# Kernel optimization log

Hardware: AMD Instinct MI355X
Metric: run time of the kernel (lower is better)

The kernel has to match this reference:

```python
import math
import jax, jax.numpy as jnp
import numpy as np

B, H, S, D = 2, 16, 2048, 64

def setup_inputs() -> dict:
    key = jax.random.key(0)
    kq, kk, kv, km = jax.random.split(key, 4)
    q = jax.random.normal(kq, (B, H, S, D), dtype=jnp.float32)
    k = jax.random.normal(kk, (B, H, S, D), dtype=jnp.float32)
    v = jax.random.normal(kv, (B, H, S, D), dtype=jnp.float32)
    mask = jax.random.randint(km, (B, S, S), 0, 2, dtype=jnp.int32)
    return {"q": q, "k": k, "v": v, "mask": mask}

def reference(q, k, v, mask):
    # attn = q @ (k^T / sqrt(d))  -> [B,H,Sq,Sk]
    scale = 1.0 / math.sqrt(q.shape[-1])
    attn = jnp.einsum("bhqd,bhkd->bhqk", q, k * scale)
    # masked_fill where mask.unsqueeze(1) == 1
    attn = jnp.where(mask[:, None, :, :] == 1, jnp.float32(-1e9), attn)
    attn = jax.nn.softmax(attn, axis=-1)
    # dropout is identity in eval / p=0
    res = jnp.einsum("bhqk,bhkd->bhqd", attn, v)
    return (res, attn)
```

## Files before the change

kernel.cpp:

```cpp
#include <hip/hip_runtime.h>

#define B_ 2
#define H_ 16
#define S_ 2048
#define D_ 64
#define QB 32
#define KT 64
#define NT (S_ / KT)
#define NTHREADS 512

typedef _Float16 f16;
typedef _Float16 f16x8 __attribute__((ext_vector_type(8)));
typedef _Float16 f16x4 __attribute__((ext_vector_type(4)));
typedef _Float16 f16x2 __attribute__((ext_vector_type(2)));
typedef float f32x4 __attribute__((ext_vector_type(4)));

#define MFMA16(a, b, c) __builtin_amdgcn_mfma_f32_16x16x32_f16(a, b, c, 0, 0, 0)

__global__ __launch_bounds__(NTHREADS)
void attn_kernel(const float* __restrict__ q, const float* __restrict__ k,
                 const float* __restrict__ v, const int* __restrict__ mask,
                 float* __restrict__ out)
{
    __shared__ f16 Qsh[QB][D_ + 8];
    __shared__ f16 Ksh[2][KT][D_ + 8];
    __shared__ f16 Vt [2][D_][KT + 8];
    __shared__ f16 Psh[2][QB][KT + 8];
    __shared__ float rowred[QB];
    __shared__ float rlsh[QB];

    const int tid  = threadIdx.x;
    const int wave = tid >> 6;
    const int lane = tid & 63;
    const int quad = lane >> 4;
    const int l16  = lane & 15;
    const int qi   = wave & 1;
    const int ni   = wave >> 1;

    const int qb = blockIdx.x;
    const int h  = blockIdx.y;
    const int b  = blockIdx.z;
    const int bh = b * H_ + h;

    const float* Qg = q + ((size_t)bh * S_ + (size_t)qb * QB) * D_;
    const float* Kg = k + (size_t)bh * S_ * D_;
    const float* Vg = v + (size_t)bh * S_ * D_;
    const int*   Mg = mask + ((size_t)b * S_ + (size_t)qb * QB) * S_;
    float* res_out  = out + ((size_t)bh * S_ + (size_t)qb * QB) * D_;
    float* attn_out = out + (size_t)B_ * H_ * S_ * D_
                          + ((size_t)bh * S_ + (size_t)qb * QB) * S_;

    if (tid < QB) rowred[tid] = 0.f;

    {
        const int row = tid >> 4;
        const int c4  = (tid & 15) * 4;
        const float4 qv = *(const float4*)(Qg + row * D_ + c4);
        f16x4 o;
        o[0] = (f16)(qv.x * 0.125f); o[1] = (f16)(qv.y * 0.125f);
        o[2] = (f16)(qv.z * 0.125f); o[3] = (f16)(qv.w * 0.125f);
        *(f16x4*)&Qsh[row][c4] = o;
    }

    const int skk = tid >> 3;
    const int sd0 = (tid & 7) * 8;
    const int vkp = tid & 31;
    const int vd0 = (tid >> 5) * 4;

    const int qrow0   = qi * 16 + quad * 4;
    const int colbase = ni * 16 + l16;
    const int* mp0 = Mg + (size_t)qrow0 * S_ + colbase;

    {
        const float* src = Kg + (size_t)skk * D_ + sd0;
        const float4 x0 = *(const float4*)(src);
        const float4 x1 = *(const float4*)(src + 4);
        f16x8 o;
        o[0] = (f16)x0.x; o[1] = (f16)x0.y; o[2] = (f16)x0.z; o[3] = (f16)x0.w;
        o[4] = (f16)x1.x; o[5] = (f16)x1.y; o[6] = (f16)x1.z; o[7] = (f16)x1.w;
        *(f16x8*)&Ksh[0][skk][sd0] = o;
    }
    int mnext[4];
#pragma unroll
    for (int r = 0; r < 4; ++r) mnext[r] = mp0[(size_t)r * S_];
    __syncthreads();

    const f16x8 a0 = *(const f16x8*)&Qsh[qi * 16 + l16][quad * 8];
    const f16x8 a1 = *(const f16x8*)&Qsh[qi * 16 + l16][32 + quad * 8];

    float psum[4] = {0.f, 0.f, 0.f, 0.f};
    for (int kt = 0; kt < NT; ++kt) {
        const int cur = kt & 1;
        const int ktn = (kt + 1 < NT) ? kt + 1 : kt;
        const float* srck = Kg + ((size_t)(ktn * KT + skk)) * D_ + sd0;
        const float4 x0 = *(const float4*)(srck);
        const float4 x1 = *(const float4*)(srck + 4);
        int mcur[4];
#pragma unroll
        for (int r = 0; r < 4; ++r) mcur[r] = mnext[r];
        const int* mpn = mp0 + ktn * KT;
#pragma unroll
        for (int r = 0; r < 4; ++r) mnext[r] = mpn[(size_t)r * S_];

        const f16x8 b0 = *(const f16x8*)&Ksh[cur][ni * 16 + l16][quad * 8];
        const f16x8 b1 = *(const f16x8*)&Ksh[cur][ni * 16 + l16][32 + quad * 8];
        f32x4 c = {0.f, 0.f, 0.f, 0.f};
        c = MFMA16(a0, b0, c);
        c = MFMA16(a1, b1, c);
#pragma unroll
        for (int r = 0; r < 4; ++r)
            psum[r] += (mcur[r] == 1) ? 0.f : __expf(c[r]);

        {
            f16x8 o;
            o[0] = (f16)x0.x; o[1] = (f16)x0.y; o[2] = (f16)x0.z; o[3] = (f16)x0.w;
            o[4] = (f16)x1.x; o[5] = (f16)x1.y; o[6] = (f16)x1.z; o[7] = (f16)x1.w;
            *(f16x8*)&Ksh[cur ^ 1][skk][sd0] = o;
        }
        __syncthreads();
    }

#pragma unroll
    for (int r = 0; r < 4; ++r) {
        psum[r] += __shfl_xor(psum[r], 1);
        psum[r] += __shfl_xor(psum[r], 2);
        psum[r] += __shfl_xor(psum[r], 4);
        psum[r] += __shfl_xor(psum[r], 8);
    }
    if (l16 == 0) {
#pragma unroll
        for (int r = 0; r < 4; ++r) atomicAdd(&rowred[qrow0 + r], psum[r]);
    }
    __syncthreads();
    if (tid < QB) rlsh[tid] = 1.0f / rowred[tid];
    __syncthreads();
    float rlq[4];
#pragma unroll
    for (int r = 0; r < 4; ++r) rlq[r] = rlsh[qrow0 + r];

    {
        const float* srck = Kg + (size_t)skk * D_ + sd0;
        const float4 x0 = *(const float4*)(srck);
        const float4 x1 = *(const float4*)(srck + 4);
        f16x8 o;
        o[0] = (f16)x0.x; o[1] = (f16)x0.y; o[2] = (f16)x0.z; o[3] = (f16)x0.w;
        o[4] = (f16)x1.x; o[5] = (f16)x1.y; o[6] = (f16)x1.z; o[7] = (f16)x1.w;
        *(f16x8*)&Ksh[0][skk][sd0] = o;

        const float* srcv = Vg + (size_t)(2 * vkp) * D_ + vd0;
        const float4 y0 = *(const float4*)(srcv);
        const float4 y1 = *(const float4*)(srcv + D_);
#pragma unroll
        for (int j = 0; j < 4; ++j) {
            f16x2 pr;
            pr[0] = (f16)((&y0.x)[j]);
            pr[1] = (f16)((&y1.x)[j]);
            *(f16x2*)&Vt[0][vd0 + j][2 * vkp] = pr;
        }
#pragma unroll
        for (int r = 0; r < 4; ++r) mnext[r] = mp0[(size_t)r * S_];
    }
    __syncthreads();

    f32x4 oacc = {0.f, 0.f, 0.f, 0.f};
    float* ap0 = attn_out + (size_t)qrow0 * S_ + colbase;
    const int dcol = colbase;

    for (int kt = 0; kt < NT; ++kt) {
        const int cur = kt & 1;
        const int nxt = cur ^ 1;
        const int ktn = (kt + 1 < NT) ? kt + 1 : kt;

        const float* srck = Kg + ((size_t)(ktn * KT + skk)) * D_ + sd0;
        const float4 x0 = *(const float4*)(srck);
        const float4 x1 = *(const float4*)(srck + 4);
        const float* srcv = Vg + ((size_t)(ktn * KT + 2 * vkp)) * D_ + vd0;
        const float4 y0 = *(const float4*)(srcv);
        const float4 y1 = *(const float4*)(srcv + D_);
        int mcur[4];
#pragma unroll
        for (int r = 0; r < 4; ++r) mcur[r] = mnext[r];
        const int* mpn = mp0 + ktn * KT;
#pragma unroll
        for (int r = 0; r < 4; ++r) mnext[r] = mpn[(size_t)r * S_];

        const f16x8 b0 = *(const f16x8*)&Ksh[cur][ni * 16 + l16][quad * 8];
        const f16x8 b1 = *(const f16x8*)&Ksh[cur][ni * 16 + l16][32 + quad * 8];
        f32x4 c = {0.f, 0.f, 0.f, 0.f};
        c = MFMA16(a0, b0, c);
        c = MFMA16(a1, b1, c);
        float* ap = ap0 + kt * KT;
#pragma unroll
        for (int r = 0; r < 4; ++r) {
            const float e = (mcur[r] == 1) ? 0.f : __expf(c[r]);
            const float p = e * rlq[r];
            ap[(size_t)r * S_] = p;
            Psh[cur][qrow0 + r][colbase] = (f16)p;
        }
        __syncthreads();

        const f16x8 pa0 = *(const f16x8*)&Psh[cur][qi * 16 + l16][quad * 8];
        const f16x8 pa1 = *(const f16x8*)&Psh[cur][qi * 16 + l16][32 + quad * 8];
        const f16x8 vb0 = *(const f16x8*)&Vt[cur][dcol][quad * 8];
        const f16x8 vb1 = *(const f16x8*)&Vt[cur][dcol][32 + quad * 8];
        oacc = MFMA16(pa0, vb0, oacc);
        oacc = MFMA16(pa1, vb1, oacc);

        {
            f16x8 o;
            o[0] = (f16)x0.x; o[1] = (f16)x0.y; o[2] = (f16)x0.z; o[3] = (f16)x0.w;
            o[4] = (f16)x1.x; o[5] = (f16)x1.y; o[6] = (f16)x1.z; o[7] = (f16)x1.w;
            *(f16x8*)&Ksh[nxt][skk][sd0] = o;
        }
#pragma unroll
        for (int j = 0; j < 4; ++j) {
            f16x2 pr;
            pr[0] = (f16)((&y0.x)[j]);
            pr[1] = (f16)((&y1.x)[j]);
            *(f16x2*)&Vt[nxt][vd0 + j][2 * vkp] = pr;
        }
        __syncthreads();
    }

#pragma unroll
    for (int r = 0; r < 4; ++r)
        res_out[(size_t)(qrow0 + r) * D_ + ni * 16 + l16] = oacc[r];
}

extern "C" void kernel_launch(void* const* d_in, const int* in_sizes, int n_in,
                              void* d_out, int out_size, void* d_ws, size_t ws_size,
                              hipStream_t stream) {
    (void)in_sizes; (void)n_in; (void)out_size; (void)d_ws; (void)ws_size;
    const float* q   = (const float*)d_in[0];
    const float* k   = (const float*)d_in[1];
    const float* v   = (const float*)d_in[2];
    const int*  mask = (const int*)d_in[3];
    float* out = (float*)d_out;
    dim3 grid(S_ / QB, H_, B_);
    attn_kernel<<<grid, dim3(NTHREADS), 0, stream>>>(q, k, v, mask, out);
}
```

Before: 933.8 us.

## Load K directly into registers in pass one and restructure pass-two pipeline

The first pass, which computes the row-sum, now has each wave load its K fragment straight from global memory into MFMA operand registers. This removes the shared-memory staging and the per-tile barrier. The second pass drops the K and P double buffers: it stages K and V from prefetched registers at the top of each iteration and keeps two barriers per tile. The shared-memory row padding shrinks from 8 to 4 halves. The trade-off is redundant global reads of K in pass one, since each wave reloads the same K rows, plus possible bank-conflict changes from the new padding.

```diff
diff --git a/kernel.cpp b/kernel.cpp
--- a/kernel.cpp
+++ b/kernel.cpp
@@ -8,10 +8,10 @@
 #define KT 64
 #define NT (S_ / KT)
 #define NTHREADS 512
+#define KP 4
 
 typedef _Float16 f16;
 typedef _Float16 f16x8 __attribute__((ext_vector_type(8)));
-typedef _Float16 f16x4 __attribute__((ext_vector_type(4)));
 typedef _Float16 f16x2 __attribute__((ext_vector_type(2)));
 typedef float f32x4 __attribute__((ext_vector_type(4)));
 
@@ -22,10 +22,10 @@
                  const float* __restrict__ v, const int* __restrict__ mask,
                  float* __restrict__ out)
 {
-    __shared__ f16 Qsh[QB][D_ + 8];
-    __shared__ f16 Ksh[2][KT][D_ + 8];
-    __shared__ f16 Vt [2][D_][KT + 8];
-    __shared__ f16 Psh[2][QB][KT + 8];
+    __shared__ f16 Qsh[QB][D_ + KP];
+    __shared__ f16 Ksh[KT][D_ + KP];
+    __shared__ f16 Vt [2][D_][KT + KP];
+    __shared__ f16 Psh[QB][KT + KP];
     __shared__ float rowred[QB];
     __shared__ float rlsh[QB];
 
@@ -52,72 +52,53 @@
 
     if (tid < QB) rowred[tid] = 0.f;
 
-    {
-        const int row = tid >> 4;
-        const int c4  = (tid & 15) * 4;
-        const float4 qv = *(const float4*)(Qg + row * D_ + c4);
-        f16x4 o;
-        o[0] = (f16)(qv.x * 0.125f); o[1] = (f16)(qv.y * 0.125f);
-        o[2] = (f16)(qv.z * 0.125f); o[3] = (f16)(qv.w * 0.125f);
-        *(f16x4*)&Qsh[row][c4] = o;
-    }
-
-    const int skk = tid >> 3;
-    const int sd0 = (tid & 7) * 8;
-    const int vkp = tid & 31;
-    const int vd0 = (tid >> 5) * 4;
+    if (tid < 256) {
+        const int row = tid >> 3;
+        const int c   = (tid & 7) * 8;
+        const float4 q0 = *(const float4*)(Qg + row * D_ + c);
+        const float4 q1 = *(const float4*)(Qg + row * D_ + c + 4);
+        f16x8 o;
+        o[0] = (f16)(q0.x * 0.125f); o[1] = (f16)(q0.y * 0.125f);
+        o[2] = (f16)(q0.z * 0.125f); o[3] = (f16)(q0.w * 0.125f);
+        o[4] = (f16)(q1.x * 0.125f); o[5] = (f16)(q1.y * 0.125f);
+        o[6] = (f16)(q1.z * 0.125f); o[7] = (f16)(q1.w * 0.125f);
+        *(f16x8*)&Qsh[row][c] = o;
+    }
+    __syncthreads();
+
+    const f16x8 a0 = *(const f16x8*)&Qsh[qi * 16 + l16][quad * 8];
+    const f16x8 a1 = *(const f16x8*)&Qsh[qi * 16 + l16][32 + quad * 8];
 
     const int qrow0   = qi * 16 + quad * 4;
     const int colbase = ni * 16 + l16;
     const int* mp0 = Mg + (size_t)qrow0 * S_ + colbase;
 
+    float psum[4] = {0.f, 0.f, 0.f, 0.f};
     {
-        const float* src = Kg + (size_t)skk * D_ + sd0;
-        const float4 x0 = *(const float4*)(src);
-        const float4 x1 = *(const float4*)(src + 4);
-        f16x8 o;
-        o[0] = (f16)x0.x; o[1] = (f16)x0.y; o[2] = (f16)x0.z; o[3] = (f16)x0.w;
-        o[4] = (f16)x1.x; o[5] = (f16)x1.y; o[6] = (f16)x1.z; o[7] = (f16)x1.w;
-        *(f16x8*)&Ksh[0][skk][sd0] = o;
-    }
-    int mnext[4];
-#pragma unroll
-    for (int r = 0; r < 4; ++r) mnext[r] = mp0[(size_t)r * S_];
-    __syncthreads();
-
-    const f16x8 a0 = *(const f16x8*)&Qsh[qi * 16 + l16][quad * 8];
-    const f16x8 a1 = *(const f16x8*)&Qsh[qi * 16 + l16][32 + quad * 8];
-
-    float psum[4] = {0.f, 0.f, 0.f, 0.f};
-    for (int kt = 0; kt < NT; ++kt) {
-        const int cur = kt & 1;
-        const int ktn = (kt + 1 < NT) ? kt + 1 : kt;
-        const float* srck = Kg + ((size_t)(ktn * KT + skk)) * D_ + sd0;
-        const float4 x0 = *(const float4*)(srck);
-        const float4 x1 = *(const float4*)(srck + 4);
-        int mcur[4];
-#pragma unroll
-        for (int r = 0; r < 4; ++r) mcur[r] = mnext[r];
-        const int* mpn = mp0 + ktn * KT;
-#pragma unroll
-        for (int r = 0; r < 4; ++r) mnext[r] = mpn[(size_t)r * S_];
-
-        const f16x8 b0 = *(const f16x8*)&Ksh[cur][ni * 16 + l16][quad * 8];
-        const f16x8 b1 = *(const f16x8*)&Ksh[cur][ni * 16 + l16][32 + quad * 8];
-        f32x4 c = {0.f, 0.f, 0.f, 0.f};
-        c = MFMA16(a0, b0, c);
-        c = MFMA16(a1, b1, c);
-#pragma unroll
-        for (int r = 0; r < 4; ++r)
-            psum[r] += (mcur[r] == 1) ? 0.f : __expf(c[r]);
-
-        {
-            f16x8 o;
-            o[0] = (f16)x0.x; o[1] = (f16)x0.y; o[2] = (f16)x0.z; o[3] = (f16)x0.w;
-            o[4] = (f16)x1.x; o[5] = (f16)x1.y; o[6] = (f16)x1.z; o[7] = (f16)x1.w;
-            *(f16x8*)&Ksh[cur ^ 1][skk][sd0] = o;
-        }
-        __syncthreads();
+        const float* kr0 = Kg + (size_t)(ni * 16 + l16) * D_;
+#pragma unroll 2
+        for (int kt = 0; kt < NT; ++kt) {
+            const float* kr = kr0 + (size_t)kt * KT * D_;
+            const float4 x0 = *(const float4*)(kr + quad * 8);
+            const float4 x1 = *(const float4*)(kr + quad * 8 + 4);
+            const float4 x2 = *(const float4*)(kr + 32 + quad * 8);
+            const float4 x3 = *(const float4*)(kr + 32 + quad * 8 + 4);
+            const int* mp = mp0 + kt * KT;
+            int m[4];
+#pragma unroll
+            for (int r = 0; r < 4; ++r) m[r] = mp[(size_t)r * S_];
+            f16x8 b0, b1;
+            b0[0] = (f16)x0.x; b0[1] = (f16)x0.y; b0[2] = (f16)x0.z; b0[3] = (f16)x0.w;
+            b0[4] = (f16)x1.x; b0[5] = (f16)x1.y; b0[6] = (f16)x1.z; b0[7] = (f16)x1.w;
+            b1[0] = (f16)x2.x; b1[1] = (f16)x2.y; b1[2] = (f16)x2.z; b1[3] = (f16)x2.w;
+            b1[4] = (f16)x3.x; b1[5] = (f16)x3.y; b1[6] = (f16)x3.z; b1[7] = (f16)x3.w;
+            f32x4 c = {0.f, 0.f, 0.f, 0.f};
+            c = MFMA16(a0, b0, c);
+            c = MFMA16(a1, b1, c);
+#pragma unroll
+            for (int r = 0; r < 4; ++r)
+                psum[r] += (m[r] == 1) ? 0.f : __expf(c[r]);
+        }
     }
 
 #pragma unroll
@@ -138,45 +119,56 @@
 #pragma unroll
     for (int r = 0; r < 4; ++r) rlq[r] = rlsh[qrow0 + r];
 
+    const int skk = tid >> 3;
+    const int sd0 = (tid & 7) * 8;
+    const int vkp = tid & 31;
+    const int vd0 = (tid >> 5) * 4;
+
+    float4 kx0, kx1, vy0, vy1;
+    int mnext[4];
     {
         const float* srck = Kg + (size_t)skk * D_ + sd0;
-        const float4 x0 = *(const float4*)(srck);
-        const float4 x1 = *(const float4*)(srck + 4);
-        f16x8 o;
-        o[0] = (f16)x0.x; o[1] = (f16)x0.y; o[2] = (f16)x0.z; o[3] = (f16)x0.w;
-        o[4] = (f16)x1.x; o[5] = (f16)x1.y; o[6] = (f16)x1.z; o[7] = (f16)x1.w;
-        *(f16x8*)&Ksh[0][skk][sd0] = o;
-
+        kx0 = *(const float4*)(srck);
+        kx1 = *(const float4*)(srck + 4);
         const float* srcv = Vg + (size_t)(2 * vkp) * D_ + vd0;
-        const float4 y0 = *(const float4*)(srcv);
-        const float4 y1 = *(const float4*)(srcv + D_);
+        vy0 = *(const float4*)(srcv);
+        vy1 = *(const float4*)(srcv + D_);
+#pragma unroll
+        for (int r = 0; r < 4; ++r) mnext[r] = mp0[(size_t)r * S_];
+    }
+
+    f32x4 oacc = {0.f, 0.f, 0.f, 0.f};
+    float* ap0 = attn_out + (size_t)qrow0 * S_ + colbase;
+
+    for (int kt = 0; kt < NT; ++kt) {
+        const int buf = kt & 1;
+        const int ktn = (kt + 1 < NT) ? kt + 1 : kt;
+
+        {
+            f16x8 o;
+            o[0] = (f16)kx0.x; o[1] = (f16)kx0.y; o[2] = (f16)kx0.z; o[3] = (f16)kx0.w;
+            o[4] = (f16)kx1.x; o[5] = (f16)kx1.y; o[6] = (f16)kx1.z; o[7] = (f16)kx1.w;
+            *(f16x8*)&Ksh[skk][sd0] = o;
+        }
 #pragma unroll
         for (int j = 0; j < 4; ++j) {
             f16x2 pr;
-            pr[0] = (f16)((&y0.x)[j]);
-            pr[1] = (f16)((&y1.x)[j]);
-            *(f16x2*)&Vt[0][vd0 + j][2 * vkp] = pr;
-        }
-#pragma unroll
-        for (int r = 0; r < 4; ++r) mnext[r] = mp0[(size_t)r * S_];
-    }
-    __syncthreads();
-
-    f32x4 oacc = {0.f, 0.f, 0.f, 0.f};
-    float* ap0 = attn_out + (size_t)qrow0 * S_ + colbase;
-    const int dcol = colbase;
-
-    for (int kt = 0; kt < NT; ++kt) {
-        const int cur = kt & 1;
-        const int nxt = cur ^ 1;
-        const int ktn = (kt + 1 < NT) ? kt + 1 : kt;
-
-        const float* srck = Kg + ((size_t)(ktn * KT + skk)) * D_ + sd0;
-        const float4 x0 = *(const float4*)(srck);
-        const float4 x1 = *(const float4*)(srck + 4);
-        const float* srcv = Vg + ((size_t)(ktn * KT + 2 * vkp)) * D_ + vd0;
-        const float4 y0 = *(const float4*)(srcv);
-        const float4 y1 = *(const float4*)(srcv + D_);
+            pr[0] = (f16)((&vy0.x)[j]);
+            pr[1] = (f16)((&vy1.x)[j]);
+            *(f16x2*)&Vt[buf][vd0 + j][2 * vkp] = pr;
+        }
+        __syncthreads();
+
+        const f16x8 b0 = *(const f16x8*)&Ksh[ni * 16 + l16][quad * 8];
+        const f16x8 b1 = *(const f16x8*)&Ksh[ni * 16 + l16][32 + quad * 8];
+        {
+            const float* srck = Kg + ((size_t)(ktn * KT + skk)) * D_ + sd0;
+            kx0 = *(const float4*)(srck);
+            kx1 = *(const float4*)(srck + 4);
+            const float* srcv = Vg + ((size_t)(ktn * KT + 2 * vkp)) * D_ + vd0;
+            vy0 = *(const float4*)(srcv);
+            vy1 = *(const float4*)(srcv + D_);
+        }
         int mcur[4];
 #pragma unroll
         for (int r = 0; r < 4; ++r) mcur[r] = mnext[r];
@@ -184,8 +176,6 @@
 #pragma unroll
         for (int r = 0; r < 4; ++r) mnext[r] = mpn[(size_t)r * S_];
 
-        const f16x8 b0 = *(const f16x8*)&Ksh[cur][ni * 16 + l16][quad * 8];
-        const f16x8 b1 = *(const f16x8*)&Ksh[cur][ni * 16 + l16][32 + quad * 8];
         f32x4 c = {0.f, 0.f, 0.f, 0.f};
         c = MFMA16(a0, b0, c);
         c = MFMA16(a1, b1, c);
@@ -195,36 +185,21 @@
             const float e = (mcur[r] == 1) ? 0.f : __expf(c[r]);
             const float p = e * rlq[r];
             ap[(size_t)r * S_] = p;
-            Psh[cur][qrow0 + r][colbase] = (f16)p;
+            Psh[qrow0 + r][colbase] = (f16)p;
         }
         __syncthreads();
 
-        const f16x8 pa0 = *(const f16x8*)&Psh[cur][qi * 16 + l16][quad * 8];
-        const f16x8 pa1 = *(const f16x8*)&Psh[cur][qi * 16 + l16][32 + quad * 8];
-        const f16x8 vb0 = *(const f16x8*)&Vt[cur][dcol][quad * 8];
-        const f16x8 vb1 = *(const f16x8*)&Vt[cur][dcol][32 + quad * 8];
+        const f16x8 pa0 = *(const f16x8*)&Psh[qi * 16 + l16][quad * 8];
+        const f16x8 pa1 = *(const f16x8*)&Psh[qi * 16 + l16][32 + quad * 8];
+        const f16x8 vb0 = *(const f16x8*)&Vt[buf][colbase][quad * 8];
+        const f16x8 vb1 = *(const f16x8*)&Vt[buf][colbase][32 + quad * 8];
         oacc = MFMA16(pa0, vb0, oacc);
         oacc = MFMA16(pa1, vb1, oacc);
-
-        {
-            f16x8 o;
-            o[0] = (f16)x0.x; o[1] = (f16)x0.y; o[2] = (f16)x0.z; o[3] = (f16)x0.w;
-            o[4] = (f16)x1.x; o[5] = (f16)x1.y; o[6] = (f16)x1.z; o[7] = (f16)x1.w;
-            *(f16x8*)&Ksh[nxt][skk][sd0] = o;
-        }
-#pragma unroll
-        for (int j = 0; j < 4; ++j) {
-            f16x2 pr;
-            pr[0] = (f16)((&y0.x)[j]);
-            pr[1] = (f16)((&y1.x)[j]);
-            *(f16x2*)&Vt[nxt][vd0 + j][2 * vkp] = pr;
-        }
-        __syncthreads();
     }
 
 #pragma unroll
     for (int r = 0; r < 4; ++r)
-        res_out[(size_t)(qrow0 + r) * D_ + ni * 16 + l16] = oacc[r];
+        res_out[(size_t)(qrow0 + r) * D_ + colbase] = oacc[r];
 }
 
 extern "C" void kernel_launch(void* const* d_in, const int* in_sizes, int n_in,
```

After: 976.6 us. 4.6% more time.

## Transpose MFMA operands so P stays in registers, swizzle block order

Applied to the files above, without the earlier changes.

Swaps the MFMA operand order so each lane holds four consecutive key columns of one query row. The mask can then be read as an int4, attention probabilities written as float4, and P fed straight into 16x16x16 MFMAs against V without staging through shared memory. Each wave now owns a disjoint slice of keys and computes partial outputs for all 64 head dims, which are summed across waves through shared memory at the end. The grid is flattened and block ids are swizzled so neighbouring blocks share the same batch mask and heads. This removes one barrier per tile and the P shared-memory buffer, but adds MFMA work for PV and a final cross-wave reduction.

```diff
diff --git a/kernel.cpp b/kernel.cpp
--- a/kernel.cpp
+++ b/kernel.cpp
@@ -8,6 +8,7 @@
 #define KT 64
 #define NT (S_ / KT)
 #define NTHREADS 512
+#define KP 4
 
 typedef _Float16 f16;
 typedef _Float16 f16x8 __attribute__((ext_vector_type(8)));
@@ -15,51 +16,62 @@
 typedef _Float16 f16x2 __attribute__((ext_vector_type(2)));
 typedef float f32x4 __attribute__((ext_vector_type(4)));
 
-#define MFMA16(a, b, c) __builtin_amdgcn_mfma_f32_16x16x32_f16(a, b, c, 0, 0, 0)
+#define MFMA32(a, b, c) __builtin_amdgcn_mfma_f32_16x16x32_f16(a, b, c, 0, 0, 0)
+#define MFMA16(a, b, c) __builtin_amdgcn_mfma_f32_16x16x16f16(a, b, c, 0, 0, 0)
+
+__device__ __forceinline__ f16x8 pack8(const float4 x0, const float4 x1) {
+    f16x8 o;
+    o[0] = (f16)x0.x; o[1] = (f16)x0.y; o[2] = (f16)x0.z; o[3] = (f16)x0.w;
+    o[4] = (f16)x1.x; o[5] = (f16)x1.y; o[6] = (f16)x1.z; o[7] = (f16)x1.w;
+    return o;
+}
 
 __global__ __launch_bounds__(NTHREADS)
 void attn_kernel(const float* __restrict__ q, const float* __restrict__ k,
                  const float* __restrict__ v, const int* __restrict__ mask,
                  float* __restrict__ out)
 {
-    __shared__ f16 Qsh[QB][D_ + 8];
-    __shared__ f16 Ksh[2][KT][D_ + 8];
-    __shared__ f16 Vt [2][D_][KT + 8];
-    __shared__ f16 Psh[2][QB][KT + 8];
+    __shared__ __align__(16) f16 KVt[2][2][KT][D_ + KP];
     __shared__ float rowred[QB];
     __shared__ float rlsh[QB];
 
     const int tid  = threadIdx.x;
+    const int lane = tid & 63;
     const int wave = tid >> 6;
-    const int lane = tid & 63;
     const int quad = lane >> 4;
     const int l16  = lane & 15;
     const int qi   = wave & 1;
     const int ni   = wave >> 1;
 
-    const int qb = blockIdx.x;
-    const int h  = blockIdx.y;
-    const int b  = blockIdx.z;
+    const int bid = blockIdx.x;
+    const int bsw = ((bid & 7) << 8) | (bid >> 3);
+    const int qb = bsw & 63;
+    const int h  = (bsw >> 6) & 15;
+    const int b  = bsw >> 10;
     const int bh = b * H_ + h;
 
     const float* Qg = q + ((size_t)bh * S_ + (size_t)qb * QB) * D_;
     const float* Kg = k + (size_t)bh * S_ * D_;
     const float* Vg = v + (size_t)bh * S_ * D_;
-    const int*   Mg = mask + ((size_t)b * S_ + (size_t)qb * QB) * S_;
     float* res_out  = out + ((size_t)bh * S_ + (size_t)qb * QB) * D_;
     float* attn_out = out + (size_t)B_ * H_ * S_ * D_
                           + ((size_t)bh * S_ + (size_t)qb * QB) * S_;
 
-    if (tid < QB) rowred[tid] = 0.f;
-
-    {
-        const int row = tid >> 4;
-        const int c4  = (tid & 15) * 4;
-        const float4 qv = *(const float4*)(Qg + row * D_ + c4);
-        f16x4 o;
-        o[0] = (f16)(qv.x * 0.125f); o[1] = (f16)(qv.y * 0.125f);
-        o[2] = (f16)(qv.z * 0.125f); o[3] = (f16)(qv.w * 0.125f);
-        *(f16x4*)&Qsh[row][c4] = o;
+    const int* mpl = mask + (size_t)b * S_ * S_
+                   + (size_t)(qb * QB + qi * 16 + l16) * S_ + ni * 16 + quad * 4;
+    float* aprow = attn_out + (size_t)(qi * 16 + l16) * S_ + ni * 16 + quad * 4;
+
+    f16x8 a0, a1;
+    {
+        const float* qrow = Qg + (size_t)(qi * 16 + l16) * D_;
+        const float4 q0 = *(const float4*)(qrow + quad * 8);
+        const float4 q1 = *(const float4*)(qrow + quad * 8 + 4);
+        const float4 q2 = *(const float4*)(qrow + 32 + quad * 8);
+        const float4 q3 = *(const float4*)(qrow + 32 + quad * 8 + 4);
+        a0[0]=(f16)(q0.x*0.125f); a0[1]=(f16)(q0.y*0.125f); a0[2]=(f16)(q0.z*0.125f); a0[3]=(f16)(q0.w*0.125f);
+        a0[4]=(f16)(q1.x*0.125f); a0[5]=(f16)(q1.y*0.125f); a0[6]=(f16)(q1.z*0.125f); a0[7]=(f16)(q1.w*0.125f);
+        a1[0]=(f16)(q2.x*0.125f); a1[1]=(f16)(q2.y*0.125f); a1[2]=(f16)(q2.z*0.125f); a1[3]=(f16)(q2.w*0.125f);
+        a1[4]=(f16)(q3.x*0.125f); a1[5]=(f16)(q3.y*0.125f); a1[6]=(f16)(q3.z*0.125f); a1[7]=(f16)(q3.w*0.125f);
     }
 
     const int skk = tid >> 3;
@@ -67,108 +79,64 @@
     const int vkp = tid & 31;
     const int vd0 = (tid >> 5) * 4;
 
-    const int qrow0   = qi * 16 + quad * 4;
-    const int colbase = ni * 16 + l16;
-    const int* mp0 = Mg + (size_t)qrow0 * S_ + colbase;
-
-    {
-        const float* src = Kg + (size_t)skk * D_ + sd0;
-        const float4 x0 = *(const float4*)(src);
-        const float4 x1 = *(const float4*)(src + 4);
-        f16x8 o;
-        o[0] = (f16)x0.x; o[1] = (f16)x0.y; o[2] = (f16)x0.z; o[3] = (f16)x0.w;
-        o[4] = (f16)x1.x; o[5] = (f16)x1.y; o[6] = (f16)x1.z; o[7] = (f16)x1.w;
-        *(f16x8*)&Ksh[0][skk][sd0] = o;
-    }
-    int mnext[4];
-#pragma unroll
-    for (int r = 0; r < 4; ++r) mnext[r] = mp0[(size_t)r * S_];
-    __syncthreads();
-
-    const f16x8 a0 = *(const f16x8*)&Qsh[qi * 16 + l16][quad * 8];
-    const f16x8 a1 = *(const f16x8*)&Qsh[qi * 16 + l16][32 + quad * 8];
-
-    float psum[4] = {0.f, 0.f, 0.f, 0.f};
+    {
+        const float* srck = Kg + (size_t)skk * D_ + sd0;
+        *(f16x8*)&KVt[0][0][skk][sd0] =
+            pack8(*(const float4*)srck, *(const float4*)(srck + 4));
+    }
+    if (tid < QB) rowred[tid] = 0.f;
+    __syncthreads();
+
+    float psum = 0.f;
     for (int kt = 0; kt < NT; ++kt) {
         const int cur = kt & 1;
         const int ktn = (kt + 1 < NT) ? kt + 1 : kt;
         const float* srck = Kg + ((size_t)(ktn * KT + skk)) * D_ + sd0;
         const float4 x0 = *(const float4*)(srck);
         const float4 x1 = *(const float4*)(srck + 4);
-        int mcur[4];
-#pragma unroll
-        for (int r = 0; r < 4; ++r) mcur[r] = mnext[r];
-        const int* mpn = mp0 + ktn * KT;
-#pragma unroll
-        for (int r = 0; r < 4; ++r) mnext[r] = mpn[(size_t)r * S_];
-
-        const f16x8 b0 = *(const f16x8*)&Ksh[cur][ni * 16 + l16][quad * 8];
-        const f16x8 b1 = *(const f16x8*)&Ksh[cur][ni * 16 + l16][32 + quad * 8];
+        const int4 mm = *(const int4*)(mpl + kt * KT);
+
+        const f16x8 b0 = *(const f16x8*)&KVt[0][cur][ni * 16 + l16][quad * 8];
+        const f16x8 b1 = *(const f16x8*)&KVt[0][cur][ni * 16 + l16][32 + quad * 8];
         f32x4 c = {0.f, 0.f, 0.f, 0.f};
-        c = MFMA16(a0, b0, c);
-        c = MFMA16(a1, b1, c);
-#pragma unroll
-        for (int r = 0; r < 4; ++r)
-            psum[r] += (mcur[r] == 1) ? 0.f : __expf(c[r]);
-
-        {
-            f16x8 o;
-            o[0] = (f16)x0.x; o[1] = (f16)x0.y; o[2] = (f16)x0.z; o[3] = (f16)x0.w;
-            o[4] = (f16)x1.x; o[5] = (f16)x1.y; o[6] = (f16)x1.z; o[7] = (f16)x1.w;
-            *(f16x8*)&Ksh[cur ^ 1][skk][sd0] = o;
-        }
+        c = MFMA32(b0, a0, c);
+        c = MFMA32(b1, a1, c);
+        psum += (mm.x == 1) ? 0.f : __expf(c[0]);
+        psum += (mm.y == 1) ? 0.f : __expf(c[1]);
+        psum += (mm.z == 1) ? 0.f : __expf(c[2]);
+        psum += (mm.w == 1) ? 0.f : __expf(c[3]);
+
+        *(f16x8*)&KVt[0][cur ^ 1][skk][sd0] = pack8(x0, x1);
         __syncthreads();
     }
-
-#pragma unroll
-    for (int r = 0; r < 4; ++r) {
-        psum[r] += __shfl_xor(psum[r], 1);
-        psum[r] += __shfl_xor(psum[r], 2);
-        psum[r] += __shfl_xor(psum[r], 4);
-        psum[r] += __shfl_xor(psum[r], 8);
-    }
-    if (l16 == 0) {
-#pragma unroll
-        for (int r = 0; r < 4; ++r) atomicAdd(&rowred[qrow0 + r], psum[r]);
-    }
+    psum += __shfl_xor(psum, 16);
+    psum += __shfl_xor(psum, 32);
+    if (lane < 16) atomicAdd(&rowred[qi * 16 + l16], psum);
     __syncthreads();
     if (tid < QB) rlsh[tid] = 1.0f / rowred[tid];
     __syncthreads();
-    float rlq[4];
-#pragma unroll
-    for (int r = 0; r < 4; ++r) rlq[r] = rlsh[qrow0 + r];
+    const float rl = rlsh[qi * 16 + l16];
 
     {
         const float* srck = Kg + (size_t)skk * D_ + sd0;
-        const float4 x0 = *(const float4*)(srck);
-        const float4 x1 = *(const float4*)(srck + 4);
-        f16x8 o;
-        o[0] = (f16)x0.x; o[1] = (f16)x0.y; o[2] = (f16)x0.z; o[3] = (f16)x0.w;
-        o[4] = (f16)x1.x; o[5] = (f16)x1.y; o[6] = (f16)x1.z; o[7] = (f16)x1.w;
-        *(f16x8*)&Ksh[0][skk][sd0] = o;
-
+        *(f16x8*)&KVt[0][0][skk][sd0] =
+            pack8(*(const float4*)srck, *(const float4*)(srck + 4));
         const float* srcv = Vg + (size_t)(2 * vkp) * D_ + vd0;
         const float4 y0 = *(const float4*)(srcv);
         const float4 y1 = *(const float4*)(srcv + D_);
 #pragma unroll
         for (int j = 0; j < 4; ++j) {
-            f16x2 pr;
-            pr[0] = (f16)((&y0.x)[j]);
-            pr[1] = (f16)((&y1.x)[j]);
-            *(f16x2*)&Vt[0][vd0 + j][2 * vkp] = pr;
+            f16x2 pr; pr[0] = (f16)((&y0.x)[j]); pr[1] = (f16)((&y1.x)[j]);
+            *(f16x2*)&KVt[1][0][vd0 + j][2 * vkp] = pr;
         }
-#pragma unroll
-        for (int r = 0; r < 4; ++r) mnext[r] = mp0[(size_t)r * S_];
-    }
-    __syncthreads();
-
-    f32x4 oacc = {0.f, 0.f, 0.f, 0.f};
-    float* ap0 = attn_out + (size_t)qrow0 * S_ + colbase;
-    const int dcol = colbase;
+    }
+    __syncthreads();
+
+    f32x4 oacc0 = {0.f,0.f,0.f,0.f}, oacc1 = {0.f,0.f,0.f,0.f};
+    f32x4 oacc2 = {0.f,0.f,0.f,0.f}, oacc3 = {0.f,0.f,0.f,0.f};
 
     for (int kt = 0; kt < NT; ++kt) {
         const int cur = kt & 1;
-        const int nxt = cur ^ 1;
         const int ktn = (kt + 1 < NT) ? kt + 1 : kt;
 
         const float* srck = Kg + ((size_t)(ktn * KT + skk)) * D_ + sd0;
@@ -177,54 +145,60 @@
         const float* srcv = Vg + ((size_t)(ktn * KT + 2 * vkp)) * D_ + vd0;
         const float4 y0 = *(const float4*)(srcv);
         const float4 y1 = *(const float4*)(srcv + D_);
-        int mcur[4];
+        const int4 mm = *(const int4*)(mpl + kt * KT);
+
+        const f16x8 b0 = *(const f16x8*)&KVt[0][cur][ni * 16 + l16][quad * 8];
+        const f16x8 b1 = *(const f16x8*)&KVt[0][cur][ni * 16 + l16][32 + quad * 8];
+        f32x4 c = {0.f, 0.f, 0.f, 0.f};
+        c = MFMA32(b0, a0, c);
+        c = MFMA32(b1, a1, c);
+        const float p0 = (mm.x == 1) ? 0.f : __expf(c[0]) * rl;
+        const float p1 = (mm.y == 1) ? 0.f : __expf(c[1]) * rl;
+        const float p2 = (mm.z == 1) ? 0.f : __expf(c[2]) * rl;
+        const float p3 = (mm.w == 1) ? 0.f : __expf(c[3]) * rl;
+        *(float4*)(aprow + (size_t)kt * KT) = make_float4(p0, p1, p2, p3);
+
+        f16x4 pb;
+        pb[0] = (f16)p0; pb[1] = (f16)p1; pb[2] = (f16)p2; pb[3] = (f16)p3;
+
+        const f16x4 vb0 = *(const f16x4*)&KVt[1][cur][ 0 + l16][ni * 16 + quad * 4];
+        const f16x4 vb1 = *(const f16x4*)&KVt[1][cur][16 + l16][ni * 16 + quad * 4];
+        const f16x4 vb2 = *(const f16x4*)&KVt[1][cur][32 + l16][ni * 16 + quad * 4];
+        const f16x4 vb3 = *(const f16x4*)&KVt[1][cur][48 + l16][ni * 16 + quad * 4];
+        oacc0 = MFMA16(vb0, pb, oacc0);
+        oacc1 = MFMA16(vb1, pb, oacc1);
+        oacc2 = MFMA16(vb2, pb, oacc2);
+        oacc3 = MFMA16(vb3, pb, oacc3);
+
+        *(f16x8*)&KVt[0][cur ^ 1][skk][sd0] = pack8(x0, x1);
 #pragma unroll
-        for (int r = 0; r < 4; ++r) mcur[r] = mnext[r];
-        const int* mpn = mp0 + ktn * KT;
-#pragma unroll
-        for (int r = 0; r < 4; ++r) mnext[r] = mpn[(size_t)r * S_];
-
-        const f16x8 b0 = *(const f16x8*)&Ksh[cur][ni * 16 + l16][quad * 8];
-        const f16x8 b1 = *(const f16x8*)&Ksh[cur][ni * 16 + l16][32 + quad * 8];
-        f32x4 c = {0.f, 0.f, 0.f, 0.f};
-        c = MFMA16(a0, b0, c);
-        c = MFMA16(a1, b1, c);
-        float* ap = ap0 + kt * KT;
-#pragma unroll
-        for (int r = 0; r < 4; ++r) {
-            const float e = (mcur[r] == 1) ? 0.f : __expf(c[r]);
-            const float p = e * rlq[r];
-            ap[(size_t)r * S_] = p;
-            Psh[cur][qrow0 + r][colbase] = (f16)p;
+        for (int j = 0; j < 4; ++j) {
+            f16x2 pr; pr[0] = (f16)((&y0.x)[j]); pr[1] = (f16)((&y1.x)[j]);
+            *(f16x2*)&KVt[1][cur ^ 1][vd0 + j][2 * vkp] = pr;
         }
         __syncthreads();
-
-        const f16x8 pa0 = *(const f16x8*)&Psh[cur][qi * 16 + l16][quad * 8];
-        const f16x8 pa1 = *(const f16x8*)&Psh[cur][qi * 16 + l16][32 + quad * 8];
-        const f16x8 vb0 = *(const f16x8*)&Vt[cur][dcol][quad * 8];
-        const f16x8 vb1 = *(const f16x8*)&Vt[cur][dcol][32 + quad * 8];
-        oacc = MFMA16(pa0, vb0, oacc);
-        oacc = MFMA16(pa1, vb1, oacc);
-
-        {
-            f16x8 o;
-            o[0] = (f16)x0.x; o[1] = (f16)x0.y; o[2] = (f16)x0.z; o[3] = (f16)x0.w;
-            o[4] = (f16)x1.x; o[5] = (f16)x1.y; o[6] = (f16)x1.z; o[7] = (f16)x1.w;
-            *(f16x8*)&Ksh[nxt][skk][sd0] = o;
-        }
-#pragma unroll
-        for (int j = 0; j < 4; ++j) {
-            f16x2 pr;
-            pr[0] = (f16)((&y0.x)[j]);
-            pr[1] = (f16)((&y1.x)[j]);
-            *(f16x2*)&Vt[nxt][vd0 + j][2 * vkp] = pr;
-        }
-        __syncthreads();
-    }
-
-#pragma unroll
-    for (int r = 0; r < 4; ++r)
-        res_out[(size_t)(qrow0 + r) * D_ + ni * 16 + l16] = oacc[r];
+    }
+
+    float* O = (float*)&KVt[0][0][0][0];
+    {
+        const int base = ((ni * 2 + qi) * 16 + l16) * 68 + quad * 4;
+        *(f32x4*)&O[base +  0] = oacc0;
+        *(f32x4*)&O[base + 16] = oacc1;
+        *(f32x4*)&O[base + 32] = oacc2;
+        *(f32x4*)&O[base + 48] = oacc3;
+    }
+    __syncthreads();
+    {
+        const int qi2 = tid >> 8;
+        const int q2  = (tid >> 4) & 15;
+        const int dc  = tid & 15;
+        const int off = (qi2 * 16 + q2) * 68 + dc * 4;
+        f32x4 s = *(f32x4*)&O[0 * 2176 + off];
+        s = s + *(f32x4*)&O[1 * 2176 + off];
+        s = s + *(f32x4*)&O[2 * 2176 + off];
+        s = s + *(f32x4*)&O[3 * 2176 + off];
+        *(f32x4*)(res_out + (size_t)(qi2 * 16 + q2) * D_ + dc * 4) = s;
+    }
 }
 
 extern "C" void kernel_launch(void* const* d_in, const int* in_sizes, int n_in,
@@ -236,6 +210,5 @@
     const float* v   = (const float*)d_in[2];
     const int*  mask = (const int*)d_in[3];
     float* out = (float*)d_out;
-    dim3 grid(S_ / QB, H_, B_);
-    attn_kernel<<<grid, dim3(NTHREADS), 0, stream>>>(q, k, v, mask, out);
+    attn_kernel<<<dim3(S_ / QB * H_ * B_), dim3(NTHREADS), 0, stream>>>(q, k, v, mask, out);
 }
```

New measurement: 947.5 us. About the same (+1.5%).
